# Performance work log

Measured on AMD Instinct MI355X. Metric: run time of the kernel, lower is better.

The kernel has to match this reference:

```python
import jax, jax.numpy as jnp
import numpy as np

KERNEL_MUL = 2.0
KERNEL_NUM = 5


def setup_inputs() -> dict:
    key = jax.random.key(0)
    k1, k2 = jax.random.split(key)
    source_features = jax.random.normal(k1, (4096, 1024), dtype=jnp.float32)
    target_features = jax.random.normal(k2, (4096, 1024), dtype=jnp.float32)
    return {"source_features": source_features, "target_features": target_features}


def reference(source_features, target_features):
    n = source_features.shape[0]
    total = jnp.concatenate([source_features, target_features], axis=0)  # [L, D]
    L = total.shape[0]
    # Pairwise squared distances via gram trick (same math as sum((a-b)**2)).
    sq = jnp.sum(total * total, axis=1)  # [L]
    d2 = jnp.maximum(sq[:, None] + sq[None, :] - 2.0 * (total @ total.T), 0.0)  # [L, L]
    # Median-heuristic-style bandwidth: mean of off-diagonal distances.
    bandwidth = jnp.sum(d2) / (L * L - L)
    bandwidth = bandwidth / (KERNEL_MUL ** (KERNEL_NUM // 2))
    # Multi-bandwidth RBF kernel sum (fixed small loop over KERNEL_NUM).
    kernel = jnp.zeros_like(d2)
    for i in range(KERNEL_NUM):
        kernel = kernel + jnp.exp(-d2 / (bandwidth * (KERNEL_MUL ** i)))
    kernel = kernel / KERNEL_NUM
    ss = jnp.mean(kernel[:n, :n])
    tt = jnp.mean(kernel[n:, n:])
    st = jnp.mean(kernel[:n, n:])
    return ss + tt - 2.0 * st
```

## Files before the change

kernel.cpp:

```cpp
#include <hip/hip_runtime.h>
#include <hip/hip_bf16.h>
#include <stdint.h>


#define L_TOTAL 8192
#define D_FEAT  1024
#define N_HALF  4096
#define TILE    128
#define TTILES  64
#define NBLK    (TTILES*(TTILES+1)/2)
#define BK      32

typedef __bf16 bf16_t;
typedef __bf16 bf16x4_t __attribute__((ext_vector_type(4)));
typedef __bf16 bf16x8_t __attribute__((ext_vector_type(8)));
typedef float  f32x4_t  __attribute__((ext_vector_type(4)));

#define XB_OFF   0
#define SQ_OFF   (L_TOTAL * D_FEAT * 2)
#define COL_OFF  (SQ_OFF + L_TOTAL * 4)
#define SACC_OFF (COL_OFF + D_FEAT * 4)
#define C0_OFF   (SACC_OFF + 8)

__device__ __forceinline__ void async_ld16(void* lds, const void* g) {
  auto ldsp = (__attribute__((address_space(3))) void*)(uintptr_t)lds;
  auto gp   = (const __attribute__((address_space(1))) void*)(uintptr_t)g;
  __builtin_amdgcn_global_load_lds(gp, ldsp, 16, 0, 0);
}

extern "C" __global__ __launch_bounds__(256) void k_prep(
    const float* __restrict__ src, const float* __restrict__ tgt,
    bf16_t* __restrict__ Xb, float* __restrict__ sq, float* __restrict__ colsum)
{
  const int row = blockIdx.x;
  const int tid = threadIdx.x;
  const float* xr = (row < N_HALF) ? (src + (size_t)row * D_FEAT)
                                   : (tgt + (size_t)(row - N_HALF) * D_FEAT);
  float4 v = ((const float4*)xr)[tid];
  bf16x4_t b;
  b[0] = (bf16_t)v.x; b[1] = (bf16_t)v.y; b[2] = (bf16_t)v.z; b[3] = (bf16_t)v.w;
  float s = 0.f;
  #pragma unroll
  for (int i = 0; i < 4; ++i) { float f = (float)b[i]; s += f * f; }
  *(bf16x4_t*)(Xb + (size_t)row * D_FEAT + tid * 4) = b;

  __shared__ float red[256];
  red[tid] = s;
  __syncthreads();
  for (int off = 128; off > 0; off >>= 1) {
    if (tid < off) red[tid] += red[tid + off];
    __syncthreads();
  }
  if (tid == 0) sq[row] = red[0];
  if (row == 0) {
    for (int c = tid; c < D_FEAT; c += 256) colsum[c] = 0.f;
  }
}

extern "C" __global__ __launch_bounds__(256) void k_colsum(
    const float* __restrict__ src, const float* __restrict__ tgt,
    float* __restrict__ colsum)
{
  const int c  = blockIdx.x * 256 + threadIdx.x;
  const int r0 = blockIdx.y * 64;
  float s = 0.f;
  for (int r = 0; r < 64; ++r) {
    int row = r0 + r;
    const float* xr = (row < N_HALF) ? (src + (size_t)row * D_FEAT)
                                     : (tgt + (size_t)(row - N_HALF) * D_FEAT);
    s += xr[c];
  }
  atomicAdd(&colsum[c], s);
}

extern "C" __global__ __launch_bounds__(256) void k_bw(
    const float* __restrict__ sq, const float* __restrict__ colsum,
    float* __restrict__ c0out, double* __restrict__ S_acc)
{
  const int tid = threadIdx.x;
  double t = 0.0;
  for (int i = tid; i < L_TOTAL; i += 256) t += (double)sq[i];
  t *= 2.0 * (double)L_TOTAL;
  for (int i = tid; i < D_FEAT; i += 256) { double v = colsum[i]; t -= 2.0 * v * v; }
  __shared__ double red[256];
  red[tid] = t;
  __syncthreads();
  for (int off = 128; off > 0; off >>= 1) {
    if (tid < off) red[tid] += red[tid + off];
    __syncthreads();
  }
  if (tid == 0) {
    double sumd2 = red[0];
    double bw = sumd2 / ((double)L_TOTAL * (double)L_TOTAL - (double)L_TOTAL);
    bw = bw / 4.0;
    *c0out = (float)(1.4426950408889634 / bw);
    *S_acc = 0.0;
  }
}

extern "C" __global__ __launch_bounds__(256) void k_mmd(
    const bf16_t* __restrict__ Xb, const float* __restrict__ sq,
    const float* __restrict__ c0ptr, double* __restrict__ S_acc)
{
  __shared__ bf16_t As[TILE * BK];
  __shared__ bf16_t Bs[TILE * BK];

  const int b = blockIdx.x;
  int ti = (int)((sqrtf(8.f * (float)b + 1.f) - 1.f) * 0.5f);
  while ((ti + 1) * (ti + 2) / 2 <= b) ++ti;
  while (ti * (ti + 1) / 2 > b) --ti;
  const int tj = b - ti * (ti + 1) / 2;
  const int row0 = ti * TILE, col0 = tj * TILE;

  const int tid  = threadIdx.x;
  const int lane = tid & 63;
  const int w    = tid >> 6;
  const int wr   = w >> 1, wc = w & 1;

  f32x4_t acc[4][4] = {};

  const int srow = lane >> 2;
  const int scol = (lane & 3) * 8;

  for (int k0 = 0; k0 < D_FEAT; k0 += BK) {
    #pragma unroll
    for (int q = 0; q < 2; ++q) {
      const int ch = w * 2 + q;
      const bf16_t* gA = Xb + (size_t)(row0 + ch * 16 + srow) * D_FEAT + k0 + scol;
      const bf16_t* gB = Xb + (size_t)(col0 + ch * 16 + srow) * D_FEAT + k0 + scol;
      async_ld16(&As[ch * 512], gA);
      async_ld16(&Bs[ch * 512], gB);
    }
    __syncthreads();

    bf16x8_t af[4], bfr[4];
    const int kg = (lane >> 4) * 8;
    #pragma unroll
    for (int m = 0; m < 4; ++m)
      af[m] = *(const bf16x8_t*)&As[(wr * 64 + m * 16 + (lane & 15)) * BK + kg];
    #pragma unroll
    for (int n = 0; n < 4; ++n)
      bfr[n] = *(const bf16x8_t*)&Bs[(wc * 64 + n * 16 + (lane & 15)) * BK + kg];

    #pragma unroll
    for (int m = 0; m < 4; ++m)
      #pragma unroll
      for (int n = 0; n < 4; ++n)
        acc[m][n] = __builtin_amdgcn_mfma_f32_16x16x32_bf16(af[m], bfr[n], acc[m][n], 0, 0, 0);
    __syncthreads();
  }

  const float c0   = *c0ptr;
  const float sgn  = ((ti < TTILES / 2) == (tj < TTILES / 2)) ? 1.f : -1.f;
  const float wgt  = (ti == tj ? 1.f : 2.f) * sgn;
  float part = 0.f;
  const int colb = col0 + wc * 64 + (lane & 15);
  const int rowb = row0 + wr * 64 + (lane >> 4) * 4;
  #pragma unroll
  for (int m = 0; m < 4; ++m) {
    #pragma unroll
    for (int n = 0; n < 4; ++n) {
      const float sqj = sq[colb + n * 16];
      #pragma unroll
      for (int r = 0; r < 4; ++r) {
        const float sqi = sq[rowb + m * 16 + r];
        float d2 = sqi + sqj - 2.f * acc[m][n][r];
        d2 = fmaxf(d2, 0.f);
        const float t  = d2 * c0;
        const float e  = __builtin_amdgcn_exp2f(-0.0625f * t);
        const float e2 = e * e, e4 = e2 * e2, e8 = e4 * e4, e16 = e8 * e8;
        part += e + e2 + e4 + e8 + e16;
      }
    }
  }
  part *= wgt;

  __shared__ float red[256];
  red[tid] = part;
  __syncthreads();
  for (int off = 128; off > 0; off >>= 1) {
    if (tid < off) red[tid] += red[tid + off];
    __syncthreads();
  }
  if (tid == 0) atomicAdd(S_acc, (double)red[0]);
}

extern "C" __global__ void k_fin(const double* __restrict__ S_acc, float* __restrict__ out)
{
  out[0] = (float)(*S_acc / (5.0 * (double)N_HALF * (double)N_HALF));
}

extern "C" void kernel_launch(void* const* d_in, const int* in_sizes, int n_in,
                              void* d_out, int out_size, void* d_ws, size_t ws_size,
                              hipStream_t stream) {
  const float* src = (const float*)d_in[0];
  const float* tgt = (const float*)d_in[1];
  float* out = (float*)d_out;
  char* ws = (char*)d_ws;
  bf16_t* Xb     = (bf16_t*)(ws + XB_OFF);
  float*  sq     = (float*)(ws + SQ_OFF);
  float*  colsum = (float*)(ws + COL_OFF);
  double* S_acc  = (double*)(ws + SACC_OFF);
  float*  c0     = (float*)(ws + C0_OFF);

  k_prep  <<<L_TOTAL, 256, 0, stream>>>(src, tgt, Xb, sq, colsum);
  k_colsum<<<dim3(4, 128), 256, 0, stream>>>(src, tgt, colsum);
  k_bw    <<<1, 256, 0, stream>>>(sq, colsum, c0, S_acc);
  k_mmd   <<<NBLK, 256, 0, stream>>>(Xb, sq, c0, S_acc);
  k_fin   <<<1, 1, 0, stream>>>(S_acc, out);
}
```

Before: 197.0 us.

## Fuse prep and column-sum passes, widen GEMM K-tile with swizzled LDS, remap blocks

The bf16 conversion, row-norm and column-sum passes are merged into one kernel that reads the inputs once, and a separate zero-init kernel replaces the racy zeroing. The main Gram/RBF kernel doubles its K-step to 64 with an XOR-swizzled LDS layout to reduce bank conflicts and halve the barrier count. Block indices are permuted across eight groups to spread triangular tiles over the device. The bandwidth reduction uses 1024 threads. The fused prep kernel launches only 128 blocks, which may underfill the GPU.

```diff
diff --git a/kernel.cpp b/kernel.cpp
--- a/kernel.cpp
+++ b/kernel.cpp
@@ -9,10 +9,9 @@
 #define TILE    128
 #define TTILES  64
 #define NBLK    (TTILES*(TTILES+1)/2)
-#define BK      32
+#define BK      64
 
 typedef __bf16 bf16_t;
-typedef __bf16 bf16x4_t __attribute__((ext_vector_type(4)));
 typedef __bf16 bf16x8_t __attribute__((ext_vector_type(8)));
 typedef float  f32x4_t  __attribute__((ext_vector_type(4)));
 
@@ -28,73 +27,88 @@
   __builtin_amdgcn_global_load_lds(gp, ldsp, 16, 0, 0);
 }
 
+extern "C" __global__ __launch_bounds__(256) void k_zero(
+    float* __restrict__ colsum, double* __restrict__ S_acc)
+{
+  const int tid = threadIdx.x;
+  for (int c = tid; c < D_FEAT; c += 256) colsum[c] = 0.f;
+  if (tid == 0) *S_acc = 0.0;
+}
+
 extern "C" __global__ __launch_bounds__(256) void k_prep(
     const float* __restrict__ src, const float* __restrict__ tgt,
     bf16_t* __restrict__ Xb, float* __restrict__ sq, float* __restrict__ colsum)
 {
-  const int row = blockIdx.x;
-  const int tid = threadIdx.x;
-  const float* xr = (row < N_HALF) ? (src + (size_t)row * D_FEAT)
-                                   : (tgt + (size_t)(row - N_HALF) * D_FEAT);
-  float4 v = ((const float4*)xr)[tid];
-  bf16x4_t b;
-  b[0] = (bf16_t)v.x; b[1] = (bf16_t)v.y; b[2] = (bf16_t)v.z; b[3] = (bf16_t)v.w;
-  float s = 0.f;
-  #pragma unroll
-  for (int i = 0; i < 4; ++i) { float f = (float)b[i]; s += f * f; }
-  *(bf16x4_t*)(Xb + (size_t)row * D_FEAT + tid * 4) = b;
-
-  __shared__ float red[256];
-  red[tid] = s;
-  __syncthreads();
-  for (int off = 128; off > 0; off >>= 1) {
-    if (tid < off) red[tid] += red[tid + off];
-    __syncthreads();
-  }
-  if (tid == 0) sq[row] = red[0];
-  if (row == 0) {
-    for (int c = tid; c < D_FEAT; c += 256) colsum[c] = 0.f;
-  }
-}
-
-extern "C" __global__ __launch_bounds__(256) void k_colsum(
-    const float* __restrict__ src, const float* __restrict__ tgt,
-    float* __restrict__ colsum)
-{
-  const int c  = blockIdx.x * 256 + threadIdx.x;
-  const int r0 = blockIdx.y * 64;
-  float s = 0.f;
-  for (int r = 0; r < 64; ++r) {
-    int row = r0 + r;
+  __shared__ float cs[4][D_FEAT];
+  const int tid  = threadIdx.x;
+  const int lane = tid & 63;
+  const int w    = tid >> 6;
+  const int rbase = blockIdx.x * 64 + w * 16;
+
+  float csp[16];
+  #pragma unroll
+  for (int j = 0; j < 16; ++j) csp[j] = 0.f;
+
+  for (int i = 0; i < 16; ++i) {
+    const int row = rbase + i;
     const float* xr = (row < N_HALF) ? (src + (size_t)row * D_FEAT)
                                      : (tgt + (size_t)(row - N_HALF) * D_FEAT);
-    s += xr[c];
-  }
-  atomicAdd(&colsum[c], s);
-}
-
-extern "C" __global__ __launch_bounds__(256) void k_bw(
+    const float4* xv = (const float4*)(xr + lane * 16);
+    float4 v[4];
+    #pragma unroll
+    for (int q = 0; q < 4; ++q) v[q] = xv[q];
+
+    bf16x8_t b0, b1;
+    float s = 0.f;
+    #pragma unroll
+    for (int q = 0; q < 4; ++q) {
+      const float f0 = v[q].x, f1 = v[q].y, f2 = v[q].z, f3 = v[q].w;
+      bf16_t c0 = (bf16_t)f0, c1 = (bf16_t)f1, c2 = (bf16_t)f2, c3 = (bf16_t)f3;
+      if (q < 2) { b0[q*4+0]=c0; b0[q*4+1]=c1; b0[q*4+2]=c2; b0[q*4+3]=c3; }
+      else       { b1[(q-2)*4+0]=c0; b1[(q-2)*4+1]=c1; b1[(q-2)*4+2]=c2; b1[(q-2)*4+3]=c3; }
+      float g0=(float)c0, g1=(float)c1, g2=(float)c2, g3=(float)c3;
+      s += g0*g0 + g1*g1 + g2*g2 + g3*g3;
+      csp[q*4+0] += f0; csp[q*4+1] += f1; csp[q*4+2] += f2; csp[q*4+3] += f3;
+    }
+    bf16_t* xb = Xb + (size_t)row * D_FEAT + lane * 16;
+    *(bf16x8_t*)xb = b0;
+    *(bf16x8_t*)(xb + 8) = b1;
+
+    #pragma unroll
+    for (int off = 32; off > 0; off >>= 1) s += __shfl_down(s, off);
+    if (lane == 0) sq[row] = s;
+  }
+
+  #pragma unroll
+  for (int j = 0; j < 16; ++j) cs[w][lane * 16 + j] = csp[j];
+  __syncthreads();
+  #pragma unroll
+  for (int k = 0; k < 4; ++k) {
+    const int c = tid * 4 + k;
+    atomicAdd(&colsum[c], cs[0][c] + cs[1][c] + cs[2][c] + cs[3][c]);
+  }
+}
+
+extern "C" __global__ __launch_bounds__(1024) void k_bw(
     const float* __restrict__ sq, const float* __restrict__ colsum,
-    float* __restrict__ c0out, double* __restrict__ S_acc)
+    float* __restrict__ c0out)
 {
   const int tid = threadIdx.x;
   double t = 0.0;
-  for (int i = tid; i < L_TOTAL; i += 256) t += (double)sq[i];
+  for (int i = tid; i < L_TOTAL; i += 1024) t += (double)sq[i];
   t *= 2.0 * (double)L_TOTAL;
-  for (int i = tid; i < D_FEAT; i += 256) { double v = colsum[i]; t -= 2.0 * v * v; }
-  __shared__ double red[256];
+  if (tid < D_FEAT) { double v = colsum[tid]; t -= 2.0 * v * v; }
+  __shared__ double red[1024];
   red[tid] = t;
   __syncthreads();
-  for (int off = 128; off > 0; off >>= 1) {
+  for (int off = 512; off > 0; off >>= 1) {
     if (tid < off) red[tid] += red[tid + off];
     __syncthreads();
   }
   if (tid == 0) {
-    double sumd2 = red[0];
-    double bw = sumd2 / ((double)L_TOTAL * (double)L_TOTAL - (double)L_TOTAL);
+    double bw = red[0] / ((double)L_TOTAL * (double)L_TOTAL - (double)L_TOTAL);
     bw = bw / 4.0;
     *c0out = (float)(1.4426950408889634 / bw);
-    *S_acc = 0.0;
   }
 }
 
@@ -104,8 +118,9 @@
 {
   __shared__ bf16_t As[TILE * BK];
   __shared__ bf16_t Bs[TILE * BK];
-
-  const int b = blockIdx.x;
+  __shared__ float  red[256];
+
+  const int b = (blockIdx.x & 7) * (NBLK / 8) + (blockIdx.x >> 3);
   int ti = (int)((sqrtf(8.f * (float)b + 1.f) - 1.f) * 0.5f);
   while ((ti + 1) * (ti + 2) / 2 <= b) ++ti;
   while (ti * (ti + 1) / 2 > b) --ti;
@@ -119,34 +134,42 @@
 
   f32x4_t acc[4][4] = {};
 
-  const int srow = lane >> 2;
-  const int scol = (lane & 3) * 8;
+  const int srow = lane >> 3;
+  const int scol = ((lane & 7) ^ srow) * 8;
 
   for (int k0 = 0; k0 < D_FEAT; k0 += BK) {
     #pragma unroll
-    for (int q = 0; q < 2; ++q) {
-      const int ch = w * 2 + q;
-      const bf16_t* gA = Xb + (size_t)(row0 + ch * 16 + srow) * D_FEAT + k0 + scol;
-      const bf16_t* gB = Xb + (size_t)(col0 + ch * 16 + srow) * D_FEAT + k0 + scol;
+    for (int q = 0; q < 4; ++q) {
+      const int ch = w * 4 + q;
+      const bf16_t* gA = Xb + (size_t)(row0 + ch * 8 + srow) * D_FEAT + k0 + scol;
+      const bf16_t* gB = Xb + (size_t)(col0 + ch * 8 + srow) * D_FEAT + k0 + scol;
       async_ld16(&As[ch * 512], gA);
       async_ld16(&Bs[ch * 512], gB);
     }
     __syncthreads();
 
-    bf16x8_t af[4], bfr[4];
-    const int kg = (lane >> 4) * 8;
-    #pragma unroll
-    for (int m = 0; m < 4; ++m)
-      af[m] = *(const bf16x8_t*)&As[(wr * 64 + m * 16 + (lane & 15)) * BK + kg];
-    #pragma unroll
-    for (int n = 0; n < 4; ++n)
-      bfr[n] = *(const bf16x8_t*)&Bs[(wc * 64 + n * 16 + (lane & 15)) * BK + kg];
-
-    #pragma unroll
-    for (int m = 0; m < 4; ++m)
-      #pragma unroll
-      for (int n = 0; n < 4; ++n)
-        acc[m][n] = __builtin_amdgcn_mfma_f32_16x16x32_bf16(af[m], bfr[n], acc[m][n], 0, 0, 0);
+    bf16x8_t af[2][4], bfr[2][4];
+    #pragma unroll
+    for (int kk = 0; kk < 2; ++kk) {
+      const int slot = kk * 4 + (lane >> 4);
+      #pragma unroll
+      for (int m = 0; m < 4; ++m) {
+        const int r = wr * 64 + m * 16 + (lane & 15);
+        af[kk][m] = *(const bf16x8_t*)&As[r * BK + (slot ^ (r & 7)) * 8];
+      }
+      #pragma unroll
+      for (int n = 0; n < 4; ++n) {
+        const int r = wc * 64 + n * 16 + (lane & 15);
+        bfr[kk][n] = *(const bf16x8_t*)&Bs[r * BK + (slot ^ (r & 7)) * 8];
+      }
+    }
+    #pragma unroll
+    for (int kk = 0; kk < 2; ++kk)
+      #pragma unroll
+      for (int m = 0; m < 4; ++m)
+        #pragma unroll
+        for (int n = 0; n < 4; ++n)
+          acc[m][n] = __builtin_amdgcn_mfma_f32_16x16x32_bf16(af[kk][m], bfr[kk][n], acc[m][n], 0, 0, 0);
     __syncthreads();
   }
 
@@ -175,7 +198,6 @@
   }
   part *= wgt;
 
-  __shared__ float red[256];
   red[tid] = part;
   __syncthreads();
   for (int off = 128; off > 0; off >>= 1) {
@@ -203,9 +225,9 @@
   double* S_acc  = (double*)(ws + SACC_OFF);
   float*  c0     = (float*)(ws + C0_OFF);
 
-  k_prep  <<<L_TOTAL, 256, 0, stream>>>(src, tgt, Xb, sq, colsum);
-  k_colsum<<<dim3(4, 128), 256, 0, stream>>>(src, tgt, colsum);
-  k_bw    <<<1, 256, 0, stream>>>(sq, colsum, c0, S_acc);
-  k_mmd   <<<NBLK, 256, 0, stream>>>(Xb, sq, c0, S_acc);
-  k_fin   <<<1, 1, 0, stream>>>(S_acc, out);
-}
+  k_zero<<<1, 256, 0, stream>>>(colsum, S_acc);
+  k_prep<<<128, 256, 0, stream>>>(src, tgt, Xb, sq, colsum);
+  k_bw  <<<1, 1024, 0, stream>>>(sq, colsum, c0);
+  k_mmd <<<NBLK, 256, 0, stream>>>(Xb, sq, c0, S_acc);
+  k_fin <<<1, 1, 0, stream>>>(S_acc, out);
+}
```

Measured after the change: 214.8 us. +9.0%, slower.
